# Optimization experiments

Hardware: AMD Instinct MI355X
Metric: run time of the kernel (lower is better)

Reference implementation:

```python
import jax, jax.numpy as jnp
import numpy as np

B, T, A, H, V = 2, 512, 768, 256, 70110  # batch, frames, audio_dim, gru_hidden, vertice_dim


def setup_inputs() -> dict:
    key = jax.random.key(0)
    ks = jax.random.split(key, 16)
    def p(k, shape, s=0.05):
        return jax.random.normal(k, shape, jnp.float32) * s
    return {
        "hidden_states": p(ks[0], (B, T, A), 1.0),
        "template": p(ks[1], (B, V), 1.0),
        "vertice": p(ks[2], (B, T, V), 1.0),
        "tf_mask": jax.random.randint(ks[3], (T,), 0, 2, jnp.int32),
        # GRU layer 0: input 2*A -> H ; layer 1: H -> H (PyTorch gate order r,z,n)
        "w_ih_l0": p(ks[4], (3 * H, 2 * A)),
        "w_hh_l0": p(ks[5], (3 * H, H)),
        "b_ih_l0": p(ks[6], (3 * H,)),
        "b_hh_l0": p(ks[7], (3 * H,)),
        "w_ih_l1": p(ks[8], (3 * H, H)),
        "w_hh_l1": p(ks[9], (3 * H, H)),
        "b_ih_l1": p(ks[10], (3 * H,)),
        "b_hh_l1": p(ks[11], (3 * H,)),
        "fc_w": p(ks[12], (V, H)),
        "fc_b": p(ks[13], (V,)),
        "red_w": p(ks[14], (A, V), 0.005),
        "red_b": p(ks[15], (A,)),
    }


def gru_cell(x, h, w_ih, w_hh, b_ih, b_hh):
    # PyTorch GRUCell math, gates ordered (r, z, n)
    gi = x @ w_ih.T + b_ih
    gh = h @ w_hh.T + b_hh
    i_r, i_z, i_n = jnp.split(gi, 3, axis=-1)
    h_r, h_z, h_n = jnp.split(gh, 3, axis=-1)
    r = jax.nn.sigmoid(i_r + h_r)
    z = jax.nn.sigmoid(i_z + h_z)
    n = jnp.tanh(i_n + r * h_n)
    return (1.0 - z) * n + z * h


def reference(hidden_states, template, vertice, tf_mask,
              w_ih_l0, w_hh_l0, b_ih_l0, b_hh_l0,
              w_ih_l1, w_hh_l1, b_ih_l1, b_hh_l1,
              fc_w, fc_b, red_w, red_b):
    dt = hidden_states.dtype
    cur = template @ red_w.T + red_b            # [B, A] reduced template vertice
    h_l0 = jnp.zeros((B, H), dt)
    h_l1 = jnp.zeros((B, H), dt)

    def step(carry, xs):
        h0, h1, cur = carry
        hs_t, vert_t, tf = xs                   # [B,A], [B,V], scalar int
        x = jnp.concatenate([hs_t, cur], axis=-1)   # [B, 2A]
        h0 = gru_cell(x, h0, w_ih_l0, w_hh_l0, b_ih_l0, b_hh_l0)
        h1 = gru_cell(h0, h1, w_ih_l1, w_hh_l1, b_ih_l1, b_hh_l1)
        pred = h1 @ fc_w.T + fc_b               # [B, V]
        loss_t = jnp.mean((pred - vert_t) ** 2)  # MSE criterion
        # teacher forcing: feed GT frame when tf==1, else own prediction
        src = jnp.where(tf.astype(bool), vert_t, pred)
        cur = src @ red_w.T + red_b             # [B, A]
        return (h0, h1, cur), (pred, loss_t)

    xs = (jnp.swapaxes(hidden_states, 0, 1),    # [T,B,A]
          jnp.swapaxes(vertice, 0, 1),          # [T,B,V]
          tf_mask)                              # [T]
    _, (preds, losses) = jax.lax.scan(step, (h_l0, h_l1, cur), xs)
    vertice_out = jnp.swapaxes(preds, 0, 1)     # [B,T,V]
    loss = jnp.mean(losses)                     # sum_t loss_t / frame_num
    return vertice_out, loss
```

## Files before the change

### kernel.cpp

```cpp
#include <hip/hip_runtime.h>
#include <hip/hip_bf16.h>


#define TT 512
#define VD 70110
#define NR 1024

using bf16x8 = __attribute__((ext_vector_type(8))) short;
using f32x4  = __attribute__((ext_vector_type(4))) float;

static __device__ __forceinline__ unsigned short f2bf(float f) {
  unsigned u = __float_as_uint(f);
  u += 0x7FFFu + ((u >> 16) & 1u);
  return (unsigned short)(u >> 16);
}

__global__ __launch_bounds__(512, 1)
void bigk_merged(const float* __restrict__ A, const float* __restrict__ vert,
                 const float* __restrict__ fcw,
                 float* __restrict__ OUTG, float* __restrict__ OUTM, int CHK)
{
  __shared__ unsigned short Al[256][40];
  __shared__ unsigned short Bl[256][40];
  const int tid = threadIdx.x;
  const bool bform = (blockIdx.x == 4);
  float* C      = bform ? OUTM : OUTG;
  const int ldc = bform ? 256 : 1024;
  const int N   = bform ? 256 : 1024;
  const int n0  = bform ? 0 : blockIdx.x * 256;
  const int m0  = blockIdx.y * 256;
  const int kc0 = blockIdx.z * CHK;
  const int kc1 = min(VD, kc0 + CHK);
  const int wave = tid >> 6, lane = tid & 63;
  const int wm = wave >> 1, wn = wave & 1;
  const int kq = lane >> 4, ln = lane & 15;
  f32x4 acc[4][8] = {};
  for (int kc = kc0; kc < kc1; kc += 32) {
    __syncthreads();
    {
      const int m = tid >> 1, kh = (tid & 1) << 4;
      const float* arow = A + (long)(m0 + m) * (long)VD;
      unsigned short tmp[16] __attribute__((aligned(16)));
      if (kc + 32 <= kc1) {
        const float2* ap2 = (const float2*)(arow + kc + kh);
#pragma unroll
        for (int i = 0; i < 8; ++i) { float2 v = ap2[i]; tmp[2*i] = f2bf(v.x); tmp[2*i+1] = f2bf(v.y); }
      } else {
#pragma unroll
        for (int i = 0; i < 16; ++i) {
          int kk = kc + kh + i;
          tmp[i] = f2bf((kk < kc1) ? arow[kk] : 0.f);
        }
      }
      ((int4*)&Al[m][kh])[0] = *(int4*)&tmp[0];
      ((int4*)&Al[m][kh])[1] = *(int4*)&tmp[8];
    }
    if (!bform) {
      const int n = tid >> 1, kh = (tid & 1) << 4;
      const float* bp = vert + (long)(n0 + n) * (long)VD;
      unsigned short tmp[16] __attribute__((aligned(16)));
      if (kc + 32 <= kc1) {
        const float2* bp2 = (const float2*)(bp + kc + kh);
#pragma unroll
        for (int i = 0; i < 8; ++i) { float2 v = bp2[i]; tmp[2*i] = f2bf(v.x); tmp[2*i+1] = f2bf(v.y); }
      } else {
#pragma unroll
        for (int i = 0; i < 16; ++i) {
          int kk = kc + kh + i;
          tmp[i] = f2bf((kk < kc1) ? bp[kk] : 0.f);
        }
      }
      ((int4*)&Bl[n][kh])[0] = *(int4*)&tmp[0];
      ((int4*)&Bl[n][kh])[1] = *(int4*)&tmp[8];
    } else {
      const int n = tid & 255, kh = (tid >> 8) << 4;
      unsigned short tmp[16] __attribute__((aligned(16)));
#pragma unroll
      for (int i = 0; i < 16; ++i) {
        int kk = kc + kh + i;
        float v = 0.f;
        if (kk < kc1 && n < 256) v = fcw[(long)kk * 256 + n];
        tmp[i] = f2bf(v);
      }
      ((int4*)&Bl[n][kh])[0] = *(int4*)&tmp[0];
      ((int4*)&Bl[n][kh])[1] = *(int4*)&tmp[8];
    }
    __syncthreads();
    bf16x8 af[4], bfv[8];
#pragma unroll
    for (int i = 0; i < 4; ++i) af[i] = *(const bf16x8*)&Al[wm*64 + i*16 + ln][kq*8];
#pragma unroll
    for (int j = 0; j < 8; ++j) bfv[j] = *(const bf16x8*)&Bl[wn*128 + j*16 + ln][kq*8];
#pragma unroll
    for (int i = 0; i < 4; ++i)
#pragma unroll
      for (int j = 0; j < 8; ++j)
        acc[i][j] = __builtin_amdgcn_mfma_f32_16x16x32_bf16(af[i], bfv[j], acc[i][j], 0, 0, 0);
  }
#pragma unroll
  for (int i = 0; i < 4; ++i)
#pragma unroll
    for (int j = 0; j < 8; ++j)
#pragma unroll
      for (int r = 0; r < 4; ++r) {
        int gm = m0 + wm*64 + i*16 + kq*4 + r;
        int gn = n0 + wn*128 + j*16 + ln;
        if (gn < N) unsafeAtomicAdd(&C[(long)gm * ldc + gn], acc[i][j][r]);
      }
}

__global__ __launch_bounds__(256)
void gemv3(const float* __restrict__ redw, const float* __restrict__ tmpl,
           const float* __restrict__ fcb, float* __restrict__ extra)
{
  const int tid = threadIdx.x;
  const int a0 = blockIdx.x * 8;
  const long k0 = (long)blockIdx.y * 8764;
  const long k1 = (k0 + 8764 < (long)VD) ? (k0 + 8764) : (long)VD;
  float s[3][8] = {};
  for (long k = k0 + tid; k < k1; k += 256) {
    const float c0 = tmpl[k], c1 = tmpl[(long)VD + k], cb2 = fcb[k];
#pragma unroll
    for (int r = 0; r < 8; ++r) {
      const float w = redw[(long)(a0 + r) * VD + k];
      s[0][r] += c0 * w; s[1][r] += c1 * w; s[2][r] += cb2 * w;
    }
  }
#pragma unroll
  for (int v = 0; v < 3; ++v)
#pragma unroll
    for (int r = 0; r < 8; ++r) {
      float x = s[v][r];
#pragma unroll
      for (int o = 32; o > 0; o >>= 1) x += __shfl_down(x, o);
      if ((tid & 63) == 0) unsafeAtomicAdd(&extra[v * 768 + a0 + r], x);
    }
}

static __device__ __forceinline__ void transpose_body(
    const float* src, int lds, float* dst, int ldd,
    int rows, int cols, const float* bias, int bx, int by)
{
  __shared__ float tile[32][33];
  const int rb = bx * 32, cb = by * 32;
  const int tx = threadIdx.x & 31, ty = threadIdx.x >> 5;
  for (int yy = ty; yy < 32; yy += 8) {
    int c = cb + yy, r = rb + tx;
    tile[yy][tx] = (c < cols && r < rows) ? src[(long)c * lds + r] : 0.f;
  }
  __syncthreads();
  for (int yy = ty; yy < 32; yy += 8) {
    int r = rb + yy, c = cb + tx;
    if (r < rows && c < cols)
      dst[(long)r * ldd + c] = tile[tx][yy] + (bias ? bias[c] : 0.f);
  }
}

__global__ void transpose_merged(const float* __restrict__ OUTG,
                                 const float* __restrict__ OUTM,
                                 const float* __restrict__ extra,
                                 const float* __restrict__ redb,
                                 float* __restrict__ GF, float* __restrict__ MT)
{
  if (blockIdx.z == 0) {
    transpose_body(OUTG, 1024, GF, 768, 1024, 768, redb, blockIdx.x, blockIdx.y);
  } else {
    if (blockIdx.x < 8) {
      transpose_body(OUTM, 256, MT, 768, 256, 768, nullptr, blockIdx.x, blockIdx.y);
    } else if (blockIdx.x == 8 && blockIdx.y == 0) {
      for (int i = threadIdx.x; i < 3 * 768; i += 256) {
        const int b = i / 768, a = i - b * 768;
        GF[(long)(1024 + b) * 768 + a] = extra[i] + redb[a];
      }
    }
  }
}

__global__ __launch_bounds__(256, 2)
void gemm128x3(const float* __restrict__ hs, const float* __restrict__ wih0,
               float* __restrict__ GIHS, const float* __restrict__ bih0,
               const float* __restrict__ GF, float* __restrict__ PM,
               const float* __restrict__ MT, float* __restrict__ M2)
{
  const float *A, *B, *bias = nullptr; float* C;
  int lda, ldb, M, N, K; long ldc;
  if (blockIdx.z == 0) {
    if (blockIdx.x >= 8) return;
    A = hs; lda = 768; B = wih0; ldb = 1536; C = GIHS; ldc = 768; bias = bih0;
    M = 1024; N = 768; K = 768;
  } else if (blockIdx.z == 1) {
    A = GF; lda = 768; B = wih0 + 768; ldb = 1536; C = PM; ldc = 768;
    M = 1027; N = 768; K = 768;
  } else {
    if (blockIdx.x >= 6 || blockIdx.y >= 2) return;
    A = wih0 + 768; lda = 1536; B = MT; ldb = 768; C = M2; ldc = 256;
    M = 768; N = 256; K = 768;
  }
  __shared__ unsigned short Al[128][40];
  __shared__ unsigned short Bl[128][40];
  const int tid = threadIdx.x;
  const int m0 = blockIdx.x * 128, n0 = blockIdx.y * 128;
  const int wave = tid >> 6, lane = tid & 63;
  const int wm = wave >> 1, wn = wave & 1;
  const int kq = lane >> 4, ln = lane & 15;
  f32x4 acc[4][4] = {};
  for (int kc = 0; kc < K; kc += 32) {
    __syncthreads();
    {
      const int m = tid >> 1, kh = (tid & 1) << 4;
      unsigned short tmp[16] __attribute__((aligned(16)));
      const bool mok = (m0 + m) < M;
      if (mok) {
        const float4* ap4 = (const float4*)(A + (long)(m0 + m) * lda + kc + kh);
#pragma unroll
        for (int i = 0; i < 4; ++i) {
          float4 v = ap4[i];
          tmp[4*i+0] = f2bf(v.x); tmp[4*i+1] = f2bf(v.y);
          tmp[4*i+2] = f2bf(v.z); tmp[4*i+3] = f2bf(v.w);
        }
      } else {
#pragma unroll
        for (int i = 0; i < 16; ++i) tmp[i] = 0;
      }
      ((int4*)&Al[m][kh])[0] = *(int4*)&tmp[0];
      ((int4*)&Al[m][kh])[1] = *(int4*)&tmp[8];
      const int n = m;
      unsigned short tmb[16] __attribute__((aligned(16)));
      const bool nok = (n0 + n) < N;
      if (nok) {
        const float4* bp4 = (const float4*)(B + (long)(n0 + n) * ldb + kc + kh);
#pragma unroll
        for (int i = 0; i < 4; ++i) {
          float4 v = bp4[i];
          tmb[4*i+0] = f2bf(v.x); tmb[4*i+1] = f2bf(v.y);
          tmb[4*i+2] = f2bf(v.z); tmb[4*i+3] = f2bf(v.w);
        }
      } else {
#pragma unroll
        for (int i = 0; i < 16; ++i) tmb[i] = 0;
      }
      ((int4*)&Bl[n][kh])[0] = *(int4*)&tmb[0];
      ((int4*)&Bl[n][kh])[1] = *(int4*)&tmb[8];
    }
    __syncthreads();
    bf16x8 af[4], bfv[4];
#pragma unroll
    for (int i = 0; i < 4; ++i) af[i]  = *(const bf16x8*)&Al[wm*64 + i*16 + ln][kq*8];
#pragma unroll
    for (int j = 0; j < 4; ++j) bfv[j] = *(const bf16x8*)&Bl[wn*64 + j*16 + ln][kq*8];
#pragma unroll
    for (int i = 0; i < 4; ++i)
#pragma unroll
      for (int j = 0; j < 4; ++j)
        acc[i][j] = __builtin_amdgcn_mfma_f32_16x16x32_bf16(af[i], bfv[j], acc[i][j], 0, 0, 0);
  }
#pragma unroll
  for (int i = 0; i < 4; ++i)
#pragma unroll
    for (int j = 0; j < 4; ++j)
#pragma unroll
      for (int r = 0; r < 4; ++r) {
        const int gm = m0 + wm*64 + i*16 + kq*4 + r;
        const int gn = n0 + wn*64 + j*16 + ln;
        if (gm < M && gn < N) {
          float v = acc[i][j][r];
          if (bias) v += bias[gn];
          C[(long)gm * ldc + gn] = v;
        }
      }
}

struct ProdLds {
  float wq[24][260], wh0s[24][260], wi1s[24][260], wh1s[24][260];
  float h0c[2][256], h1c[2][256];
  float dotsS[2][2][3][8];
  int tfl[TT];
};
struct ConsLds {
  unsigned short As[128][264];
  unsigned short Bl[128][40];
  float wred[8];
};

#define HALF_DOTS(W, H, MS)                                                   \
  {                                                                           \
    const int g8_ = tid >> 3, l8_ = tid & 7;                                  \
    if (g8_ < 48) {                                                           \
      const int row_ = g8_ >> 1, bb_ = g8_ & 1;                               \
      const float4* w4_ = (const float4*)&(W)[row_][0];                       \
      const float4* h4_ = (const float4*)&(H)[bb_][0];                        \
      float s_ = 0.f;                                                         \
      _Pragma("unroll")                                                       \
      for (int i = 0; i < 8; ++i) {                                           \
        const float4 a_ = w4_[i * 8 + l8_], h_ = h4_[i * 8 + l8_];            \
        s_ += a_.x * h_.x + a_.y * h_.y + a_.z * h_.z + a_.w * h_.w;          \
      }                                                                       \
      s_ += __shfl_xor(s_, 1); s_ += __shfl_xor(s_, 2); s_ += __shfl_xor(s_, 4); \
      if (l8_ == 0) dotsS[MS][bb_][row_ >> 3][row_ & 7] = s_;                 \
    }                                                                         \
  }

#define POLL_ISSUE(buf, var)                                                  \
  unsigned long long var = __hip_atomic_load(&(buf)[tid], __ATOMIC_RELAXED, __HIP_MEMORY_SCOPE_AGENT);
#define POLL_FINISH(buf, var, dstLds, want)                                   \
  {                                                                           \
    const unsigned w_ = (unsigned)(want); int sp_ = 0;                        \
    while ((unsigned)(var >> 32) < w_ && ++sp_ < (1 << 15)) {                 \
      __builtin_amdgcn_s_sleep(1);                                            \
      var = __hip_atomic_load(&(buf)[tid], __ATOMIC_RELAXED, __HIP_MEMORY_SCOPE_AGENT); \
    }                                                                         \
    ((float*)dstLds)[tid] = __uint_as_float((unsigned)var);                   \
  }
#define POLLP(buf, dstLds, want)                                              \
  { POLL_ISSUE(buf, pw_); POLL_FINISH(buf, pw_, dstLds, want); }

__global__ __launch_bounds__(512, 1)
void k3_fused(const float* __restrict__ gihs, const float* __restrict__ Pm,
              const float* __restrict__ M2m,
              const float* __restrict__ whh0, const float* __restrict__ bhh0,
              const float* __restrict__ wih1, const float* __restrict__ bih1,
              const float* __restrict__ whh1, const float* __restrict__ bhh1,
              const int* __restrict__ tfm,
              unsigned short* __restrict__ h1sb,
              unsigned long long* __restrict__ h0p, unsigned long long* __restrict__ h1p,
              unsigned* __restrict__ prog,
              const float* __restrict__ fcw, const float* __restrict__ fcb,
              const float* __restrict__ vert,
              float* __restrict__ out, float* __restrict__ lossp)
{
  __shared__ union { ProdLds p; ConsLds c; } U;
  const int tid = threadIdx.x;

  if (blockIdx.x >= 32) {
    auto& C = U.c;
    const int idx = blockIdx.x - 32;
    int tx, memb, cnt;
    if (idx < 24)      { tx = 0; memb = (idx)      >> 1; cnt = 12; }
    else if (idx < 48) { tx = 1; memb = (idx - 24) >> 1; cnt = 12; }
    else if (idx < 96) { tx = 2; memb = (idx - 48) >> 1; cnt = 24; }
    else               { tx = 3; memb = (idx - 96) >> 1; cnt = 64; }
    const int b = idx & 1;
    const int nt0 = memb * 548 / cnt, nt1 = (memb + 1) * 548 / cnt;
    if (nt0 >= nt1) return;
    const unsigned want = (unsigned)((tx + 1) * 128);
    if (tid < 32) {
      int sp = 0;
      while (__hip_atomic_load(&prog[tid * 16], __ATOMIC_RELAXED, __HIP_MEMORY_SCOPE_AGENT) < want) {
        if (++sp > (1 << 14)) break;
        for (int j = 0; j < 16; ++j) __builtin_amdgcn_s_sleep(15);
      }
    }
    __syncthreads();
    const long rbase = (long)b * 512 + (long)tx * 128;
    {
      const unsigned long long* src = (const unsigned long long*)(h1sb + rbase * 256);
#pragma unroll
      for (int i = 0; i < 16; ++i) {
        const int u = tid * 16 + i;
        unsigned long long v = __hip_atomic_load(&src[u], __ATOMIC_RELAXED, __HIP_MEMORY_SCOPE_AGENT);
        const int row = u >> 6, c4 = u & 63;
        *(unsigned long long*)&C.As[row][c4 * 4] = v;
      }
    }
    __syncthreads();
    const int wave = tid >> 6, lane = tid & 63;
    const int wm = wave >> 2, wn = wave & 3;
    const int kq = lane >> 4, ln = lane & 15;
    for (int nt = nt0; nt < nt1; ++nt) {
      const int n0 = nt * 128;
      f32x4 acc[4][2] = {};
#pragma unroll 1
      for (int ks = 0; ks < 8; ++ks) {
        __syncthreads();
        {
          const int rn = tid >> 2, kh = (tid & 3) * 8;
          const int gn = n0 + rn;
          unsigned short tmb[8] __attribute__((aligned(16)));
          if (gn < VD) {
            const float4* bp = (const float4*)&fcw[(long)gn * 256 + ks * 32 + kh];
            float4 v0 = bp[0], v1 = bp[1];
            tmb[0] = f2bf(v0.x); tmb[1] = f2bf(v0.y); tmb[2] = f2bf(v0.z); tmb[3] = f2bf(v0.w);
            tmb[4] = f2bf(v1.x); tmb[5] = f2bf(v1.y); tmb[6] = f2bf(v1.z); tmb[7] = f2bf(v1.w);
          } else {
#pragma unroll
            for (int i = 0; i < 8; ++i) tmb[i] = 0;
          }
          *(int4*)&C.Bl[rn][kh] = *(int4*)tmb;
        }
        __syncthreads();
        bf16x8 af[4], bfv[2];
#pragma unroll
        for (int i = 0; i < 4; ++i)
          af[i] = *(const bf16x8*)&C.As[wm*64 + i*16 + ln][ks*32 + kq*8];
#pragma unroll
        for (int j = 0; j < 2; ++j)
          bfv[j] = *(const bf16x8*)&C.Bl[wn*32 + j*16 + ln][kq*8];
#pragma unroll
        for (int i = 0; i < 4; ++i)
#pragma unroll
          for (int j = 0; j < 2; ++j)
            acc[i][j] = __builtin_amdgcn_mfma_f32_16x16x32_bf16(af[i], bfv[j], acc[i][j], 0, 0, 0);
      }
      float ls = 0.f;
#pragma unroll
      for (int i = 0; i < 4; ++i)
#pragma unroll
        for (int j = 0; j < 2; ++j)
#pragma unroll
          for (int r = 0; r < 4; ++r) {
            const int gmL = wm*64 + i*16 + kq*4 + r;
            const int gn = n0 + wn*32 + j*16 + ln;
            if (gn < VD) {
              const float v = acc[i][j][r] + fcb[gn];
              const long grow = rbase + gmL;
              out[grow * VD + gn] = v;
              const float dd = v - vert[grow * VD + gn];
              ls += dd * dd;
            }
          }
#pragma unroll
      for (int o = 32; o > 0; o >>= 1) ls += __shfl_down(ls, o);
      if (lane == 0) C.wred[wave] = ls;
      __syncthreads();
      if (tid == 0) {
        float s = 0.f;
#pragma unroll
        for (int w = 0; w < 8; ++w) s += C.wred[w];
        lossp[(tx * 2 + b) * 548 + nt] = s;
      }
      __syncthreads();
    }
    return;
  }

  float (&wq)[24][260]   = U.p.wq;
  float (&wh0s)[24][260] = U.p.wh0s;
  float (&wi1s)[24][260] = U.p.wi1s;
  float (&wh1s)[24][260] = U.p.wh1s;
  float (&h0c)[2][256]   = U.p.h0c;
  float (&h1c)[2][256]   = U.p.h1c;
  float (&dotsS)[2][2][3][8] = U.p.dotsS;
  int   (&tfl)[TT]       = U.p.tfl;
  const int wg = blockIdx.x;
  const int j0 = wg * 8;

  {
    const int col = tid & 255, rh = tid >> 8;
    for (int row = rh; row < 24; row += 2) {
      const int g = row >> 3, jj = row & 7;
      const long gr = g * 256 + j0 + jj;
      wq[row][col]   = M2m[gr * 256 + col];
      wh0s[row][col] = whh0[gr * 256 + col];
      wi1s[row][col] = wih1[gr * 256 + col];
      wh1s[row][col] = whh1[gr * 256 + col];
    }
  }
  ((float*)h0c)[tid] = 0.f;
  ((float*)h1c)[tid] = 0.f;
  if (tid < TT) tfl[tid] = tfm[tid];

  const int cb = tid >> 3, cjj = tid & 7, cj = j0 + cjj;
  float bh0v[3], bi1v[3], bh1v[3], d2v[3];
  if (tid < 16) {
#pragma unroll
    for (int g = 0; g < 3; ++g) {
      bh0v[g] = bhh0[g*256 + cj];
      bi1v[g] = bih1[g*256 + cj];
      bh1v[g] = bhh1[g*256 + cj];
      d2v[g]  = Pm[(long)1026 * 768 + g*256 + cj];
    }
  }
  __syncthreads();

  const int wave = tid >> 6;
  float gihsv[3], piv[3];
  if (tid < 16) {
#pragma unroll
    for (int g = 0; g < 3; ++g) {
      gihsv[g] = gihs[((long)cb * TT) * 768 + g*256 + cj];
      piv[g]   = Pm[(long)(1024 + cb) * 768 + g*256 + cj];
    }
  }
  for (int t = 0; t < TT; ++t) {
    const int tfprev = (t == 0) ? 1 : tfl[t - 1];
    if (!tfprev) {
      POLL_ISSUE(h1p + (t & 1) * 512, pb);
      HALF_DOTS(wh0s, h0c, 1);
      POLL_FINISH(h1p + (t & 1) * 512, pb, h1c, t);
      __syncthreads();
      HALF_DOTS(wq, h1c, 0);
    } else {
      HALF_DOTS(wh0s, h0c, 1);
    }
    __syncthreads();
    if (tid < 16) {
      float gi[3], gh[3];
#pragma unroll
      for (int g = 0; g < 3; ++g) {
        const float q = tfprev ? 0.f : (dotsS[0][cb][g][cjj] + d2v[g]);
        gi[g] = gihsv[g] + (tfprev ? piv[g] : q);
        gh[g] = dotsS[1][cb][g][cjj] + bh0v[g];
      }
      const float rr = 1.f / (1.f + __expf(-(gi[0] + gh[0])));
      const float zz = 1.f / (1.f + __expf(-(gi[1] + gh[1])));
      const float nn = tanhf(gi[2] + rr * gh[2]);
      const float h0n = (1.f - zz) * nn + zz * h0c[cb][cj];
      const unsigned long long pk =
          ((unsigned long long)(unsigned)(t + 1) << 32) | (unsigned long long)__float_as_uint(h0n);
      __hip_atomic_store(&h0p[((t + 1) & 1) * 512 + cb * 256 + cj], pk,
                         __ATOMIC_RELAXED, __HIP_MEMORY_SCOPE_AGENT);
    }
    if (tid < 16 && t + 1 < TT) {
#pragma unroll
      for (int g = 0; g < 3; ++g) {
        gihsv[g] = gihs[((long)cb * TT + (t + 1)) * 768 + g*256 + cj];
        piv[g]   = Pm[((long)cb * TT + t) * 768 + g*256 + cj];
      }
    }
    __syncthreads();
    POLL_ISSUE(h0p + ((t + 1) & 1) * 512, hw);
    if (tfprev) {
      POLL_ISSUE(h1p + (t & 1) * 512, qb);
      POLL_FINISH(h1p + (t & 1) * 512, qb, h1c, t);
      __syncthreads();
    }
    HALF_DOTS(wh1s, h1c, 1);
    POLL_FINISH(h0p + ((t + 1) & 1) * 512, hw, h0c, t + 1);
    __syncthreads();
    HALF_DOTS(wi1s, h0c, 0);
    __syncthreads();
    if (tid < 16) {
      float gi[3], gh[3];
#pragma unroll
      for (int g = 0; g < 3; ++g) {
        gi[g] = dotsS[0][cb][g][cjj] + bi1v[g];
        gh[g] = dotsS[1][cb][g][cjj] + bh1v[g];
      }
      const float rr = 1.f / (1.f + __expf(-(gi[0] + gh[0])));
      const float zz = 1.f / (1.f + __expf(-(gi[1] + gh[1])));
      const float nn = tanhf(gi[2] + rr * gh[2]);
      const float h1n = (1.f - zz) * nn + zz * h1c[cb][cj];
      const unsigned hb = (unsigned)f2bf(h1n);
      asm volatile("global_store_short %0, %1, off sc0 sc1"
                   :: "v"(&h1sb[((long)cb * TT + t) * 256 + cj]), "v"(hb) : "memory");
      const unsigned long long pk =
          ((unsigned long long)(unsigned)(t + 1) << 32) | (unsigned long long)__float_as_uint(h1n);
      __hip_atomic_store(&h1p[((t + 1) & 1) * 512 + cb * 256 + cj], pk,
                         __ATOMIC_RELAXED, __HIP_MEMORY_SCOPE_AGENT);
    }
    if ((t & 15) == 15) {
      if (wave == 0) asm volatile("s_waitcnt vmcnt(0)" ::: "memory");
      if (tid == 0)
        __hip_atomic_store(&prog[wg * 16], (unsigned)(t + 1),
                           __ATOMIC_RELAXED, __HIP_MEMORY_SCOPE_AGENT);
    }
    __syncthreads();
  }
}

__global__ void loss_finalize(const float* __restrict__ lossp, int n, float* __restrict__ out) {
  __shared__ float red[256];
  float s = 0.f;
  for (int i = threadIdx.x; i < n; i += 256) s += lossp[i];
  red[threadIdx.x] = s;
  __syncthreads();
  for (int st = 128; st > 0; st >>= 1) {
    if (threadIdx.x < st) red[threadIdx.x] += red[threadIdx.x + st];
    __syncthreads();
  }
  if (threadIdx.x == 0) out[0] = red[0] * (1.0f / 71792640.0f);
}

extern "C" void kernel_launch(void* const* d_in, const int* in_sizes, int n_in,
                              void* d_out, int out_size, void* d_ws, size_t ws_size,
                              hipStream_t stream) {
  (void)in_sizes; (void)n_in; (void)out_size; (void)ws_size;
  const float* hs   = (const float*)d_in[0];
  const float* tmpl = (const float*)d_in[1];
  const float* vert = (const float*)d_in[2];
  const int*   tfm  = (const int*)  d_in[3];
  const float* wih0 = (const float*)d_in[4];
  const float* whh0 = (const float*)d_in[5];
  const float* bih0 = (const float*)d_in[6];
  const float* bhh0 = (const float*)d_in[7];
  const float* wih1 = (const float*)d_in[8];
  const float* whh1 = (const float*)d_in[9];
  const float* bih1 = (const float*)d_in[10];
  const float* bhh1 = (const float*)d_in[11];
  const float* fcw  = (const float*)d_in[12];
  const float* fcb  = (const float*)d_in[13];
  const float* redw = (const float*)d_in[14];
  const float* redb = (const float*)d_in[15];
  float* out = (float*)d_out;

  char* ws = (char*)d_ws;
  float*    LOSSP = (float*)(ws + 0);
  float*    OUTG  = (float*)(ws + 0);
  float*    OUTM  = (float*)(ws + 3145728);
  float*    EXTRA = (float*)(ws + 3932160);
  unsigned long long* H0P = (unsigned long long*)(ws + 3941376);
  unsigned long long* H1P = (unsigned long long*)(ws + 3949568);
  unsigned* PROG  = (unsigned*)(ws + 3957760);
  float*    GF    = (float*)(ws + 3960064);
  float*    MT    = (float*)(ws + 7115776);
  float*    GIHS  = (float*)(ws + 7902208);
  float*    PM    = (float*)(ws + 11047936);
  float*    M2    = (float*)(ws + 14203648);
  unsigned short* H1SB = (unsigned short*)(ws + 14990080);

  hipMemsetAsync(d_ws, 0, 3960064, stream);

  bigk_merged<<<dim3(5, 3, 21), 512, 0, stream>>>(redw, vert, fcw, OUTG, OUTM, 3344);
  gemv3<<<dim3(96, 8), 256, 0, stream>>>(redw, tmpl, fcb, EXTRA);

  transpose_merged<<<dim3(32, 24, 2), 256, 0, stream>>>(OUTG, OUTM, EXTRA, redb, GF, MT);

  gemm128x3<<<dim3(9, 6, 3), 256, 0, stream>>>(hs, wih0, GIHS, bih0, GF, PM, MT, M2);

  k3_fused<<<256, 512, 0, stream>>>(GIHS, PM, M2, whh0, bhh0, wih1, bih1, whh1, bhh1,
                                    tfm, H1SB, H0P, H1P, PROG,
                                    fcw, fcb, vert, out, LOSSP);

  loss_finalize<<<1, 256, 0, stream>>>(LOSSP, 4384, out + 71792640L);
}
```

Baseline: 2.891 ms.

## Overlap half of reduce-GEMM into recurrent kernel and pre-convert fc weights to bf16

Shrinks the upfront big-K reduction GEMM to three of its five column groups. The other two (frames for the second half of the sequence) are computed inside idle consumer blocks of the fused recurrent kernel. Those blocks then transpose the result to bf16 and build the matching part of the projection matrix PM. The recurrent producer waits on a progress counter only at step 256. The fc weights are also converted to bf16 once into workspace so consumer blocks load bf16 directly. This adds spin-wait synchronisation, atomics and extra workspace, and falls back to the old path if the workspace is too small.

```diff
diff --git a/kernel.cpp b/kernel.cpp
--- a/kernel.cpp
+++ b/kernel.cpp
@@ -15,19 +15,36 @@
   return (unsigned short)(u >> 16);
 }
 
+__global__ __launch_bounds__(256)
+void tobf16(const float* __restrict__ src, unsigned short* __restrict__ dst, long n)
+{
+  const long c0 = ((long)blockIdx.x * 256 + threadIdx.x) * 8;
+  if (c0 + 8 <= n) {
+    const float2* s2 = (const float2*)(src + c0);
+    unsigned short t[8] __attribute__((aligned(16)));
+#pragma unroll
+    for (int i = 0; i < 4; ++i) { float2 v = s2[i]; t[2*i] = f2bf(v.x); t[2*i+1] = f2bf(v.y); }
+    *(int4*)(dst + c0) = *(int4*)t;
+  } else {
+    for (long c = c0; c < n; ++c) dst[c] = f2bf(src[c]);
+  }
+}
+
 __global__ __launch_bounds__(512, 1)
 void bigk_merged(const float* __restrict__ A, const float* __restrict__ vert,
                  const float* __restrict__ fcw,
-                 float* __restrict__ OUTG, float* __restrict__ OUTM, int CHK)
+                 float* __restrict__ OUTG, float* __restrict__ OUTM, int CHK, int xmap)
 {
   __shared__ unsigned short Al[256][40];
   __shared__ unsigned short Bl[256][40];
   const int tid = threadIdx.x;
-  const bool bform = (blockIdx.x == 4);
+  const int xs3[3] = {0, 2, 4};
+  const int x = xmap ? xs3[blockIdx.x] : blockIdx.x;
+  const bool bform = (x == 4);
   float* C      = bform ? OUTM : OUTG;
   const int ldc = bform ? 256 : 1024;
   const int N   = bform ? 256 : 1024;
-  const int n0  = bform ? 0 : blockIdx.x * 256;
+  const int n0  = bform ? 0 : x * 256;
   const int m0  = blockIdx.y * 256;
   const int kc0 = blockIdx.z * CHK;
   const int kc1 = min(VD, kc0 + CHK);
@@ -160,10 +177,16 @@
                                  const float* __restrict__ OUTM,
                                  const float* __restrict__ extra,
                                  const float* __restrict__ redb,
-                                 float* __restrict__ GF, float* __restrict__ MT)
+                                 float* __restrict__ GF, float* __restrict__ MT,
+                                 int s2on)
 {
   if (blockIdx.z == 0) {
-    transpose_body(OUTG, 1024, GF, 768, 1024, 768, redb, blockIdx.x, blockIdx.y);
+    int bx = blockIdx.x;
+    if (s2on) {
+      if (bx >= 16) return;
+      bx = (bx < 8) ? bx : bx + 8;
+    }
+    transpose_body(OUTG, 1024, GF, 768, 1024, 768, redb, bx, blockIdx.y);
   } else {
     if (blockIdx.x < 8) {
       transpose_body(OUTM, 256, MT, 768, 256, 768, nullptr, blockIdx.x, blockIdx.y);
@@ -180,15 +203,20 @@
 void gemm128x3(const float* __restrict__ hs, const float* __restrict__ wih0,
                float* __restrict__ GIHS, const float* __restrict__ bih0,
                const float* __restrict__ GF, float* __restrict__ PM,
-               const float* __restrict__ MT, float* __restrict__ M2)
+               const float* __restrict__ MT, float* __restrict__ M2, int s2on)
 {
   const float *A, *B, *bias = nullptr; float* C;
-  int lda, ldb, M, N, K; long ldc;
+  int lda, ldb, M, N, K; long ldc; int mblk = blockIdx.x;
   if (blockIdx.z == 0) {
     if (blockIdx.x >= 8) return;
     A = hs; lda = 768; B = wih0; ldb = 1536; C = GIHS; ldc = 768; bias = bih0;
     M = 1024; N = 768; K = 768;
   } else if (blockIdx.z == 1) {
+    if (s2on) {
+      const int tbl[5] = {0, 1, 4, 5, 8};
+      if (blockIdx.x >= 5) return;
+      mblk = tbl[blockIdx.x];
+    }
     A = GF; lda = 768; B = wih0 + 768; ldb = 1536; C = PM; ldc = 768;
     M = 1027; N = 768; K = 768;
   } else {
@@ -199,7 +227,7 @@
   __shared__ unsigned short Al[128][40];
   __shared__ unsigned short Bl[128][40];
   const int tid = threadIdx.x;
-  const int m0 = blockIdx.x * 128, n0 = blockIdx.y * 128;
+  const int m0 = mblk * 128, n0 = blockIdx.y * 128;
   const int wave = tid >> 6, lane = tid & 63;
   const int wm = wave >> 1, wn = wave & 1;
   const int kq = lane >> 4, ln = lane & 15;
@@ -280,6 +308,10 @@
   unsigned short As[128][264];
   unsigned short Bl[128][40];
   float wred[8];
+};
+struct S2Lds {
+  unsigned short Al[256][40];
+  unsigned short Bl[256][40];
 };
 
 #define HALF_DOTS(W, H, MS)                                                   \
@@ -315,7 +347,7 @@
   { POLL_ISSUE(buf, pw_); POLL_FINISH(buf, pw_, dstLds, want); }
 
 __global__ __launch_bounds__(512, 1)
-void k3_fused(const float* __restrict__ gihs, const float* __restrict__ Pm,
+void k3_fused(const float* __restrict__ gihs, const float* Pm,
               const float* __restrict__ M2m,
               const float* __restrict__ whh0, const float* __restrict__ bhh0,
               const float* __restrict__ wih1, const float* __restrict__ bih1,
@@ -324,16 +356,196 @@
               unsigned short* __restrict__ h1sb,
               unsigned long long* __restrict__ h0p, unsigned long long* __restrict__ h1p,
               unsigned* __restrict__ prog,
-              const float* __restrict__ fcw, const float* __restrict__ fcb,
-              const float* __restrict__ vert,
-              float* __restrict__ out, float* __restrict__ lossp)
+              const float* __restrict__ fcw, const unsigned short* __restrict__ FB,
+              int s2on,
+              const float* __restrict__ fcb, const float* __restrict__ vert,
+              float* __restrict__ out, float* __restrict__ lossp,
+              const float* __restrict__ redw, float* __restrict__ outg,
+              unsigned short* __restrict__ gf2b, float* pmw,
+              const float* __restrict__ redb, const float* __restrict__ wr)
 {
-  __shared__ union { ProdLds p; ConsLds c; } U;
+  __shared__ union { ProdLds p; ConsLds c; S2Lds s; } U;
   const int tid = threadIdx.x;
 
   if (blockIdx.x >= 32) {
+    const int idx = blockIdx.x - 32;
+
+    if (s2on && idx >= 96 && idx < 222) {
+      const int r2 = idx - 96;
+      {
+        auto& S = U.s;
+        const int x2 = (r2 < 63) ? 1 : 3;
+        const int rem = (r2 < 63) ? r2 : r2 - 63;
+        const int m0 = (rem / 21) * 256;
+        const int kc0 = (rem % 21) * 3344;
+        const int kc1 = min(VD, kc0 + 3344);
+        const int n0 = x2 * 256;
+        const int wave = tid >> 6, lane = tid & 63;
+        const int wm = wave >> 1, wn = wave & 1;
+        const int kq = lane >> 4, ln = lane & 15;
+        f32x4 acc[4][8] = {};
+        for (int kc = kc0; kc < kc1; kc += 32) {
+          __syncthreads();
+          {
+            const int m = tid >> 1, kh = (tid & 1) << 4;
+            const float* arow = redw + (long)(m0 + m) * (long)VD;
+            unsigned short tmp[16] __attribute__((aligned(16)));
+            if (kc + 32 <= kc1) {
+              const float2* ap2 = (const float2*)(arow + kc + kh);
+#pragma unroll
+              for (int i = 0; i < 8; ++i) { float2 v = ap2[i]; tmp[2*i] = f2bf(v.x); tmp[2*i+1] = f2bf(v.y); }
+            } else {
+#pragma unroll
+              for (int i = 0; i < 16; ++i) {
+                int kk = kc + kh + i;
+                tmp[i] = f2bf((kk < kc1) ? arow[kk] : 0.f);
+              }
+            }
+            ((int4*)&S.Al[m][kh])[0] = *(int4*)&tmp[0];
+            ((int4*)&S.Al[m][kh])[1] = *(int4*)&tmp[8];
+            const float* bp = vert + (long)(n0 + m) * (long)VD;
+            unsigned short tmb[16] __attribute__((aligned(16)));
+            if (kc + 32 <= kc1) {
+              const float2* bp2 = (const float2*)(bp + kc + kh);
+#pragma unroll
+              for (int i = 0; i < 8; ++i) { float2 v = bp2[i]; tmb[2*i] = f2bf(v.x); tmb[2*i+1] = f2bf(v.y); }
+            } else {
+#pragma unroll
+              for (int i = 0; i < 16; ++i) {
+                int kk = kc + kh + i;
+                tmb[i] = f2bf((kk < kc1) ? bp[kk] : 0.f);
+              }
+            }
+            ((int4*)&S.Bl[m][kh])[0] = *(int4*)&tmb[0];
+            ((int4*)&S.Bl[m][kh])[1] = *(int4*)&tmb[8];
+          }
+          __syncthreads();
+          bf16x8 af[4], bfv[8];
+#pragma unroll
+          for (int i = 0; i < 4; ++i) af[i] = *(const bf16x8*)&S.Al[wm*64 + i*16 + ln][kq*8];
+#pragma unroll
+          for (int j = 0; j < 8; ++j) bfv[j] = *(const bf16x8*)&S.Bl[wn*128 + j*16 + ln][kq*8];
+#pragma unroll
+          for (int i = 0; i < 4; ++i)
+#pragma unroll
+            for (int j = 0; j < 8; ++j)
+              acc[i][j] = __builtin_amdgcn_mfma_f32_16x16x32_bf16(af[i], bfv[j], acc[i][j], 0, 0, 0);
+        }
+#pragma unroll
+        for (int i = 0; i < 4; ++i)
+#pragma unroll
+          for (int j = 0; j < 8; ++j)
+#pragma unroll
+            for (int r = 0; r < 4; ++r) {
+              const int gm = m0 + wm*64 + i*16 + kq*4 + r;
+              const int gn = n0 + wn*128 + j*16 + ln;
+              unsafeAtomicAdd(&outg[(long)gm * 1024 + gn], acc[i][j][r]);
+            }
+        __syncthreads();
+        if (tid == 0)
+          (void)__hip_atomic_fetch_add(&prog[512], 1u, __ATOMIC_RELAXED, __HIP_MEMORY_SCOPE_AGENT);
+      }
+      if (r2 < 24) {
+        if (tid == 0) {
+          int sp = 0;
+          while (__hip_atomic_load(&prog[512], __ATOMIC_RELAXED, __HIP_MEMORY_SCOPE_AGENT) < 126u) {
+            if (++sp > (1 << 16)) break;
+            for (int j = 0; j < 8; ++j) __builtin_amdgcn_s_sleep(15);
+          }
+        }
+        __syncthreads();
+        const int yy = tid >> 4, pr = tid & 15;
+        for (int i = 0; i < 16; ++i) {
+          const int tt = r2 * 16 + i;
+          const int bxI = tt / 24, by = tt % 24;
+          const int bx = (bxI < 8) ? (8 + bxI) : (16 + bxI);
+          const int r = bx * 32 + yy;
+          const int c = by * 32 + pr * 2;
+          float f0 = __hip_atomic_load(&outg[(long)c * 1024 + r],
+                                       __ATOMIC_RELAXED, __HIP_MEMORY_SCOPE_AGENT);
+          float f1 = __hip_atomic_load(&outg[(long)(c + 1) * 1024 + r],
+                                       __ATOMIC_RELAXED, __HIP_MEMORY_SCOPE_AGENT);
+          const unsigned pk = (unsigned)f2bf(f0 + redb[c]) |
+                              ((unsigned)f2bf(f1 + redb[c + 1]) << 16);
+          __hip_atomic_store((unsigned*)gf2b + ((long)r * 384 + (c >> 1)), pk,
+                             __ATOMIC_RELAXED, __HIP_MEMORY_SCOPE_AGENT);
+        }
+        if (tid == 0)
+          (void)__hip_atomic_fetch_add(&prog[520], 1u, __ATOMIC_RELAXED, __HIP_MEMORY_SCOPE_AGENT);
+        if (tid == 0) {
+          int sp = 0;
+          while (__hip_atomic_load(&prog[520], __ATOMIC_RELAXED, __HIP_MEMORY_SCOPE_AGENT) < 24u) {
+            if (++sp > (1 << 16)) break;
+            for (int j = 0; j < 4; ++j) __builtin_amdgcn_s_sleep(15);
+          }
+        }
+        __syncthreads();
+        {
+          auto& S = U.s;
+          unsigned short (*Als)[40] = (unsigned short(*)[40])&S.Al[0][0];
+          unsigned short (*Bls)[40] = (unsigned short(*)[40])&S.Bl[0][0];
+          const int rowtbl[4] = {2, 3, 6, 7};
+          const int m0 = rowtbl[r2 / 6] * 128;
+          const int n0 = (r2 % 6) * 128;
+          const int wave = tid >> 6, lane = tid & 63;
+          const int wm = wave >> 2, wn = wave & 3;
+          const int kq = lane >> 4, ln = lane & 15;
+          f32x4 acc[4][2] = {};
+          for (int kc = 0; kc < 768; kc += 32) {
+            __syncthreads();
+            {
+              const unsigned* g2 = (const unsigned*)gf2b;
+#pragma unroll
+              for (int i = 0; i < 4; ++i) {
+                const int u = tid * 4 + i;
+                const int row = u >> 4, cp = u & 15;
+                unsigned v = __hip_atomic_load(&g2[(long)(m0 + row) * 384 + (kc >> 1) + cp],
+                                               __ATOMIC_RELAXED, __HIP_MEMORY_SCOPE_AGENT);
+                *(unsigned*)&Als[row][cp * 2] = v;
+              }
+#pragma unroll
+              for (int i = 0; i < 4; ++i) {
+                const int u = tid * 4 + i;
+                const int row = u >> 4, k2 = (u & 15) * 2;
+                const float2 v = *(const float2*)&wr[(long)(n0 + row) * 1536 + kc + k2];
+                const unsigned pk = (unsigned)f2bf(v.x) | ((unsigned)f2bf(v.y) << 16);
+                *(unsigned*)&Bls[row][k2] = pk;
+              }
+            }
+            __syncthreads();
+            bf16x8 af[4], bfv[2];
+#pragma unroll
+            for (int i = 0; i < 4; ++i)
+              af[i] = *(const bf16x8*)&Als[wm*64 + i*16 + ln][kq*8];
+#pragma unroll
+            for (int j = 0; j < 2; ++j)
+              bfv[j] = *(const bf16x8*)&Bls[wn*32 + j*16 + ln][kq*8];
+#pragma unroll
+            for (int i = 0; i < 4; ++i)
+#pragma unroll
+              for (int j = 0; j < 2; ++j)
+                acc[i][j] = __builtin_amdgcn_mfma_f32_16x16x32_bf16(af[i], bfv[j], acc[i][j], 0, 0, 0);
+          }
+#pragma unroll
+          for (int i = 0; i < 4; ++i)
+#pragma unroll
+            for (int j = 0; j < 2; ++j)
+#pragma unroll
+              for (int r = 0; r < 4; ++r) {
+                const int gm = m0 + wm*64 + i*16 + kq*4 + r;
+                const int gn = n0 + wn*32 + j*16 + ln;
+                __hip_atomic_store(&pmw[(long)gm * 768 + gn], acc[i][j][r],
+                                   __ATOMIC_RELAXED, __HIP_MEMORY_SCOPE_AGENT);
+              }
+        }
+        __syncthreads();
+        if (tid == 0)
+          (void)__hip_atomic_fetch_add(&prog[528], 1u, __ATOMIC_RELAXED, __HIP_MEMORY_SCOPE_AGENT);
+      }
+      __syncthreads();
+    }
+
     auto& C = U.c;
-    const int idx = blockIdx.x - 32;
     int tx, memb, cnt;
     if (idx < 24)      { tx = 0; memb = (idx)      >> 1; cnt = 12; }
     else if (idx < 48) { tx = 1; memb = (idx - 24) >> 1; cnt = 12; }
@@ -375,17 +587,23 @@
         {
           const int rn = tid >> 2, kh = (tid & 3) * 8;
           const int gn = n0 + rn;
-          unsigned short tmb[8] __attribute__((aligned(16)));
-          if (gn < VD) {
-            const float4* bp = (const float4*)&fcw[(long)gn * 256 + ks * 32 + kh];
-            float4 v0 = bp[0], v1 = bp[1];
-            tmb[0] = f2bf(v0.x); tmb[1] = f2bf(v0.y); tmb[2] = f2bf(v0.z); tmb[3] = f2bf(v0.w);
-            tmb[4] = f2bf(v1.x); tmb[5] = f2bf(v1.y); tmb[6] = f2bf(v1.z); tmb[7] = f2bf(v1.w);
+          if (s2on) {
+            int4 v = {0, 0, 0, 0};
+            if (gn < VD) v = *(const int4*)(FB + (long)gn * 256 + ks * 32 + kh);
+            *(int4*)&C.Bl[rn][kh] = v;
           } else {
-#pragma unroll
-            for (int i = 0; i < 8; ++i) tmb[i] = 0;
+            unsigned short tmb[8] __attribute__((aligned(16)));
+            if (gn < VD) {
+              const float4* bp = (const float4*)&fcw[(long)gn * 256 + ks * 32 + kh];
+              float4 v0 = bp[0], v1 = bp[1];
+              tmb[0] = f2bf(v0.x); tmb[1] = f2bf(v0.y); tmb[2] = f2bf(v0.z); tmb[3] = f2bf(v0.w);
+              tmb[4] = f2bf(v1.x); tmb[5] = f2bf(v1.y); tmb[6] = f2bf(v1.z); tmb[7] = f2bf(v1.w);
+            } else {
+#pragma unroll
+              for (int i = 0; i < 8; ++i) tmb[i] = 0;
+            }
+            *(int4*)&C.Bl[rn][kh] = *(int4*)tmb;
           }
-          *(int4*)&C.Bl[rn][kh] = *(int4*)tmb;
         }
         __syncthreads();
         bf16x8 af[4], bfv[2];
@@ -482,6 +700,16 @@
     }
   }
   for (int t = 0; t < TT; ++t) {
+    if (s2on && t == 256) {
+      if (tid == 0) {
+        int sp = 0;
+        while (__hip_atomic_load(&prog[528], __ATOMIC_RELAXED, __HIP_MEMORY_SCOPE_AGENT) < 24u) {
+          if (++sp > (1 << 18)) break;
+          __builtin_amdgcn_s_sleep(8);
+        }
+      }
+      __syncthreads();
+    }
     const int tfprev = (t == 0) ? 1 : tfl[t - 1];
     if (!tfprev) {
       POLL_ISSUE(h1p + (t & 1) * 512, pb);
@@ -574,7 +802,7 @@
 extern "C" void kernel_launch(void* const* d_in, const int* in_sizes, int n_in,
                               void* d_out, int out_size, void* d_ws, size_t ws_size,
                               hipStream_t stream) {
-  (void)in_sizes; (void)n_in; (void)out_size; (void)ws_size;
+  (void)in_sizes; (void)n_in; (void)out_size;
   const float* hs   = (const float*)d_in[0];
   const float* tmpl = (const float*)d_in[1];
   const float* vert = (const float*)d_in[2];
@@ -607,19 +835,30 @@
   float*    PM    = (float*)(ws + 11047936);
   float*    M2    = (float*)(ws + 14203648);
   unsigned short* H1SB = (unsigned short*)(ws + 14990080);
+  unsigned short* GF2B = (unsigned short*)(ws + 15514624);
+  unsigned short* FB   = (unsigned short*)(ws + 17087488);
+  LOSSP = (float*)(ws + 52983808);
+  const size_t NEEDED = 52983808UL + 4384UL * 4UL;
+  const int s2 = (ws_size >= NEEDED) ? 1 : 0;
 
   hipMemsetAsync(d_ws, 0, 3960064, stream);
 
-  bigk_merged<<<dim3(5, 3, 21), 512, 0, stream>>>(redw, vert, fcw, OUTG, OUTM, 3344);
+  if (s2) {
+    tobf16<<<dim3(8764), 256, 0, stream>>>(fcw, FB, 17948160L);
+    bigk_merged<<<dim3(3, 3, 21), 512, 0, stream>>>(redw, vert, fcw, OUTG, OUTM, 3344, 1);
+  } else {
+    bigk_merged<<<dim3(5, 3, 21), 512, 0, stream>>>(redw, vert, fcw, OUTG, OUTM, 3344, 0);
+  }
   gemv3<<<dim3(96, 8), 256, 0, stream>>>(redw, tmpl, fcb, EXTRA);
 
-  transpose_merged<<<dim3(32, 24, 2), 256, 0, stream>>>(OUTG, OUTM, EXTRA, redb, GF, MT);
-
-  gemm128x3<<<dim3(9, 6, 3), 256, 0, stream>>>(hs, wih0, GIHS, bih0, GF, PM, MT, M2);
+  transpose_merged<<<dim3(32, 24, 2), 256, 0, stream>>>(OUTG, OUTM, EXTRA, redb, GF, MT, s2);
+  gemm128x3<<<dim3(9, 6, 3), 256, 0, stream>>>(hs, wih0, GIHS, bih0, GF, PM, MT, M2, s2);
 
   k3_fused<<<256, 512, 0, stream>>>(GIHS, PM, M2, whh0, bhh0, wih1, bih1, whh1, bhh1,
                                     tfm, H1SB, H0P, H1P, PROG,
-                                    fcw, fcb, vert, out, LOSSP);
-
-  loss_finalize<<<1, 256, 0, stream>>>(LOSSP, 4384, out + 71792640L);
-}
+                                    fcw, FB, s2, fcb, vert, out,
+                                    s2 ? LOSSP : (float*)(ws + 0),
+                                    redw, OUTG, GF2B, PM, redb, wih0 + 768);
+
+  loss_finalize<<<1, 256, 0, stream>>>(s2 ? LOSSP : (float*)(ws + 0), 4384, out + 71792640L);
+}
```

After: 2.501 ms. 13.5% less time.
